# Performance work log

Hardware: AMD Instinct MI355X
Metric: run time of the kernel (lower is better)

Reference implementation:

```python
import jax, jax.numpy as jnp
import numpy as np

DIM_K = 128
MODEL_DIM = 1024
B, S = 8, 2048

def setup_inputs() -> dict:
    key = jax.random.key(0)
    k1, k2, k3, k4, k5, k6, k7 = jax.random.split(key, 7)
    return {
        "query": jax.random.normal(k1, (B, S, MODEL_DIM), dtype=jnp.float32),
        "key": jax.random.normal(k2, (B, S, MODEL_DIM), dtype=jnp.float32),
        "value": jax.random.normal(k3, (B, S, MODEL_DIM), dtype=jnp.float32),
        "mask": jax.random.randint(k4, (B, S, S), 0, 2, dtype=jnp.int32),
        # nn.Linear(model_dim, dim_k, bias=False): weight shape [dim_k, model_dim]
        "Wq": jax.random.normal(k5, (DIM_K, MODEL_DIM), dtype=jnp.float32) * (MODEL_DIM ** -0.5),
        "Wk": jax.random.normal(k6, (DIM_K, MODEL_DIM), dtype=jnp.float32) * (MODEL_DIM ** -0.5),
        "Wv": jax.random.normal(k7, (DIM_K, MODEL_DIM), dtype=jnp.float32) * (MODEL_DIM ** -0.5),
    }

def reference(query, key, value, mask, Wq, Wk, Wv):
    # projections: y = x @ W.T
    q = jnp.einsum('bsm,km->bsk', query, Wq)
    k = jnp.einsum('bsm,km->bsk', key, Wk)
    v = jnp.einsum('bsm,km->bsk', value, Wv)
    scale = 1.0 / jnp.sqrt(jnp.float32(DIM_K))
    pre_score = jnp.einsum('bqk,bsk->bqs', q, k) * scale  # [B,Sq,Sk]
    pre_score = jnp.where(mask == 0, jnp.float32(-1e9), pre_score)
    score = jax.nn.softmax(pre_score, axis=-1)
    return jnp.einsum('bqs,bsk->bqk', score, v)
```

## Files before the change

### kernel.cpp

```cpp
#include <hip/hip_runtime.h>
#include <hip/hip_bf16.h>

typedef __bf16 bf16x8 __attribute__((ext_vector_type(8)));
typedef float  f32x4  __attribute__((ext_vector_type(4)));

#define WS_Q  786432
#define WS_KP 2883584
#define WS_VP 4980736
#define WS_BF16_BYTES 14155776ull

__global__ __launch_bounds__(256) void wconv_kernel(
    const float* __restrict__ wq, const float* __restrict__ wk,
    const float* __restrict__ wv, __bf16* __restrict__ wpack)
{
    int i = blockIdx.x * 256 + threadIdx.x;
    int p = i >> 17, o = i & 131071;
    int c = o >> 3, j = o & 7;
    int l15 = c & 15, g = (c >> 4) & 3, nt = (c >> 6) & 7, ks = (c >> 9) & 1, kk = c >> 10;
    int col = nt * 16 + l15;
    int k = kk * 64 + ks * 32 + g * 8 + j;
    const float* src = (p == 0) ? wq : ((p == 1) ? wk : wv);
    float f = src[col * 1024 + k];
    if (p == 0) f *= (0.08838834764831845f * 1.44269504088896340736f);
    __bf16 h = (__bf16)f;
    __bf16 l = (__bf16)(f - (float)h);
    wpack[p * 262144 + o]          = h;
    wpack[p * 262144 + 131072 + o] = l;
}

__global__ __launch_bounds__(256, 4) void proj_kernel(
    const float* __restrict__ xq, const float* __restrict__ xk,
    const float* __restrict__ xv, const __bf16* __restrict__ wpack,
    __bf16* __restrict__ qws, __bf16* __restrict__ kpack, __bf16* __restrict__ vpack)
{
    const int p = blockIdx.y;
    const float* __restrict__ x = (p == 0) ? xq : ((p == 1) ? xk : xv);
    const __bf16* __restrict__ wf = wpack + p * 262144;

    const int mtile = blockIdx.x;
    const int m0 = mtile << 6;
    const int t = threadIdx.x;
    const int wv_ = t >> 6;
    const int lane = t & 63;
    const int l15 = lane & 15, g = lane >> 4;

    __shared__ __align__(16) __bf16 olds[9216];

    f32x4 acc[8];
#pragma unroll
    for (int nt = 0; nt < 8; ++nt) acc[nt] = (f32x4){0.f, 0.f, 0.f, 0.f};

    const float* xrow = x + (size_t)(m0 + wv_ * 16 + l15) * 1024 + g * 8;

    f32x4 a0 = *(const f32x4*)(xrow);
    f32x4 a1 = *(const f32x4*)(xrow + 4);
    f32x4 b0 = *(const f32x4*)(xrow + 32);
    f32x4 b1 = *(const f32x4*)(xrow + 36);

    for (int kk = 0; kk < 16; ++kk) {
        f32x4 na0, na1, nb0, nb1;
        if (kk < 15) {
            const float* nx = xrow + (kk + 1) * 64;
            na0 = *(const f32x4*)(nx);
            na1 = *(const f32x4*)(nx + 4);
            nb0 = *(const f32x4*)(nx + 32);
            nb1 = *(const f32x4*)(nx + 36);
        }
        bf16x8 ah0, ah1;
#pragma unroll
        for (int j = 0; j < 4; ++j) {
            ah0[j] = (__bf16)a0[j]; ah0[4 + j] = (__bf16)a1[j];
            ah1[j] = (__bf16)b0[j]; ah1[4 + j] = (__bf16)b1[j];
        }
        const __bf16* wb = wf + kk * 8192 + lane * 8;
#pragma unroll
        for (int nt = 0; nt < 8; ++nt) {
            bf16x8 bh0 = *(const bf16x8*)(wb + nt * 512);
            bf16x8 bl0 = *(const bf16x8*)(wb + nt * 512 + 131072);
            bf16x8 bh1 = *(const bf16x8*)(wb + nt * 512 + 4096);
            bf16x8 bl1 = *(const bf16x8*)(wb + nt * 512 + 4096 + 131072);
            acc[nt] = __builtin_amdgcn_mfma_f32_16x16x32_bf16(ah0, bh0, acc[nt], 0, 0, 0);
            acc[nt] = __builtin_amdgcn_mfma_f32_16x16x32_bf16(ah0, bl0, acc[nt], 0, 0, 0);
            acc[nt] = __builtin_amdgcn_mfma_f32_16x16x32_bf16(ah1, bh1, acc[nt], 0, 0, 0);
            acc[nt] = __builtin_amdgcn_mfma_f32_16x16x32_bf16(ah1, bl1, acc[nt], 0, 0, 0);
        }
        a0 = na0; a1 = na1; b0 = nb0; b1 = nb1;
    }

#pragma unroll
    for (int nt = 0; nt < 8; ++nt)
#pragma unroll
        for (int r = 0; r < 4; ++r) {
            int rowl = wv_ * 16 + g * 4 + r;
            int col = nt * 16 + l15;
            __bf16 v = (__bf16)acc[nt][r];
            if (p < 2) olds[rowl * 136 + col] = v;
            else       olds[col * 72 + rowl] = v;
        }
    __syncthreads();

    if (p == 0) {
#pragma unroll
        for (int i = 0; i < 4; ++i) {
            int idx = i * 256 + t;
            int row = idx >> 4, ck = idx & 15;
            bf16x8 v = *(const bf16x8*)(olds + row * 136 + ck * 8);
            *(bf16x8*)(qws + (size_t)(m0 + row) * 128 + ck * 8) = v;
        }
    } else if (p == 1) {
#pragma unroll
        for (int i = 0; i < 4; ++i) {
            int idx = i * 256 + t;
            int ks = idx >> 8, nt = (idx >> 6) & 3, ln = idx & 63;
            int gg = ln >> 4, ll = ln & 15;
            bf16x8 v = *(const bf16x8*)(olds + (nt * 16 + ll) * 136 + ks * 32 + gg * 8);
            *(bf16x8*)(kpack + ((size_t)mtile * 1024 + idx) * 8) = v;
        }
    } else {
#pragma unroll
        for (int i = 0; i < 4; ++i) {
            int idx = i * 256 + t;
            int ks2 = idx >> 9, nt2 = (idx >> 6) & 7, ln = idx & 63;
            int gg = ln >> 4, ll = ln & 15;
            bf16x8 v = *(const bf16x8*)(olds + (nt2 * 16 + ll) * 72 + ks2 * 32 + gg * 8);
            *(bf16x8*)(vpack + ((size_t)mtile * 1024 + idx) * 8) = v;
        }
    }
}

__global__ __launch_bounds__(256, 3) void flash_kernel(
    const __bf16* __restrict__ qws, const __bf16* __restrict__ kpack,
    const __bf16* __restrict__ vpack, const int* __restrict__ mask,
    float* __restrict__ out, float* __restrict__ part, float* __restrict__ mlbuf,
    int ktp)
{
    const int bb = blockIdx.x & 7;
    const int rest = blockIdx.x >> 3;
    const int mtile = rest & 31;
    const int jsplit = rest >> 5;
    const int sq0 = mtile << 6;
    const int t = threadIdx.x;
    const int wv_ = t >> 6;
    const int lane = t & 63;
    const int l15 = lane & 15, g = lane >> 4;

    __shared__ __align__(16) __bf16 psmem[4 * 1152];
    __bf16* plds = psmem + wv_ * 1152;

    bf16x8 qf[4];
    {
        const __bf16* qp = qws + ((size_t)(bb * 2048 + sq0 + wv_ * 16 + l15)) * 128 + g * 8;
#pragma unroll
        for (int ks = 0; ks < 4; ++ks) qf[ks] = *(const bf16x8*)(qp + ks * 32);
    }

    f32x4 o[8];
#pragma unroll
    for (int nt = 0; nt < 8; ++nt) o[nt] = (f32x4){0.f, 0.f, 0.f, 0.f};
    float m_run[4], l_run[4];
#pragma unroll
    for (int r = 0; r < 4; ++r) { m_run[r] = -__builtin_inff(); l_run[r] = 0.f; }

    const int* mbase = mask + ((size_t)(bb * 2048 + sq0 + wv_ * 16 + g * 4)) * 2048 + l15;
    const __bf16* kbase = kpack + ((size_t)(bb * 32) * 1024) * 8 + lane * 8;
    const __bf16* vbase = vpack + ((size_t)(bb * 32) * 1024) * 8 + lane * 8;

    const int kt_begin = jsplit * ktp, kt_end = kt_begin + ktp;
    for (int kt = kt_begin; kt < kt_end; ++kt) {
        const int n0 = kt << 6;

        int mv[4][4];
#pragma unroll
        for (int nt = 0; nt < 4; ++nt)
#pragma unroll
            for (int r = 0; r < 4; ++r)
                mv[nt][r] = mbase[(size_t)r * 2048 + n0 + nt * 16];

        const __bf16* kb = kbase + kt * 8192;
        f32x4 sf[4];
#pragma unroll
        for (int nt = 0; nt < 4; ++nt) sf[nt] = (f32x4){0.f, 0.f, 0.f, 0.f};
#pragma unroll
        for (int nt = 0; nt < 4; ++nt)
#pragma unroll
            for (int ks = 0; ks < 4; ++ks) {
                bf16x8 bfk = *(const bf16x8*)(kb + (ks * 4 + nt) * 512);
                sf[nt] = __builtin_amdgcn_mfma_f32_16x16x32_bf16(qf[ks], bfk, sf[nt], 0, 0, 0);
            }

        float mx[4], mnew[4], alpha[4], psum[4];
#pragma unroll
        for (int r = 0; r < 4; ++r)
            mx[r] = fmaxf(fmaxf(sf[0][r], sf[1][r]), fmaxf(sf[2][r], sf[3][r]));
#pragma unroll
        for (int off = 1; off < 16; off <<= 1)
#pragma unroll
            for (int r = 0; r < 4; ++r)
                mx[r] = fmaxf(mx[r], __shfl_xor(mx[r], off, 64));
#pragma unroll
        for (int r = 0; r < 4; ++r) {
            mnew[r] = fmaxf(m_run[r], mx[r]);
            alpha[r] = exp2f(m_run[r] - mnew[r]);
            psum[r] = 0.f;
        }
#pragma unroll
        for (int nt = 0; nt < 4; ++nt)
#pragma unroll
            for (int r = 0; r < 4; ++r) {
                float pv = exp2f(sf[nt][r] - mnew[r]);
                pv = mv[nt][r] ? pv : 0.f;
                psum[r] += pv;
                plds[(g * 4 + r) * 72 + nt * 16 + l15] = (__bf16)pv;
            }
#pragma unroll
        for (int off = 1; off < 16; off <<= 1)
#pragma unroll
            for (int r = 0; r < 4; ++r)
                psum[r] += __shfl_xor(psum[r], off, 64);
#pragma unroll
        for (int r = 0; r < 4; ++r) {
            l_run[r] = l_run[r] * alpha[r] + psum[r];
            m_run[r] = mnew[r];
        }
#pragma unroll
        for (int nt = 0; nt < 8; ++nt)
#pragma unroll
            for (int r = 0; r < 4; ++r) o[nt][r] *= alpha[r];

        bf16x8 pa[2];
#pragma unroll
        for (int ks2 = 0; ks2 < 2; ++ks2)
            pa[ks2] = *(const bf16x8*)(plds + l15 * 72 + ks2 * 32 + g * 8);

        const __bf16* vb = vbase + kt * 8192;
#pragma unroll
        for (int nt2 = 0; nt2 < 8; ++nt2)
#pragma unroll
            for (int ks2 = 0; ks2 < 2; ++ks2) {
                bf16x8 bfv = *(const bf16x8*)(vb + (ks2 * 8 + nt2) * 512);
                o[nt2] = __builtin_amdgcn_mfma_f32_16x16x32_bf16(pa[ks2], bfv, o[nt2], 0, 0, 0);
            }
    }

    if (part == nullptr) {
        float inv[4];
#pragma unroll
        for (int r = 0; r < 4; ++r) inv[r] = 1.0f / l_run[r];
#pragma unroll
        for (int nt2 = 0; nt2 < 8; ++nt2)
#pragma unroll
            for (int r = 0; r < 4; ++r)
                out[((size_t)(bb * 2048 + sq0 + wv_ * 16 + g * 4 + r)) * 128 + nt2 * 16 + l15] =
                    o[nt2][r] * inv[r];
    } else {
#pragma unroll
        for (int nt2 = 0; nt2 < 8; ++nt2)
#pragma unroll
            for (int r = 0; r < 4; ++r) {
                size_t rowg = (size_t)(bb * 2048 + sq0 + wv_ * 16 + g * 4 + r);
                part[((size_t)jsplit * 16384 + rowg) * 128 + nt2 * 16 + l15] = o[nt2][r];
            }
        if (l15 == 0) {
#pragma unroll
            for (int r = 0; r < 4; ++r) {
                size_t rowg = (size_t)(bb * 2048 + sq0 + wv_ * 16 + g * 4 + r);
                mlbuf[((size_t)jsplit * 16384 + rowg) * 2]     = m_run[r];
                mlbuf[((size_t)jsplit * 16384 + rowg) * 2 + 1] = l_run[r];
            }
        }
    }
}

__global__ __launch_bounds__(256) void merge_kernel(
    const float* __restrict__ part, const float* __restrict__ mlbuf,
    float* __restrict__ out, int J)
{
    int t = threadIdx.x;
    size_t row = (size_t)blockIdx.x * 8 + (t >> 5);
    int c = (t & 31) * 4;
    float mj[4];
    float m = -__builtin_inff();
    for (int j = 0; j < J; ++j) {
        mj[j] = mlbuf[((size_t)j * 16384 + row) * 2];
        m = fmaxf(m, mj[j]);
    }
    float l = 0.f;
    f32x4 acc = (f32x4){0.f, 0.f, 0.f, 0.f};
    for (int j = 0; j < J; ++j) {
        float w = exp2f(mj[j] - m);
        l += w * mlbuf[((size_t)j * 16384 + row) * 2 + 1];
        f32x4 v = *(const f32x4*)(part + ((size_t)j * 16384 + row) * 128 + c);
#pragma unroll
        for (int e = 0; e < 4; ++e) acc[e] += w * v[e];
    }
    float inv = 1.0f / l;
#pragma unroll
    for (int e = 0; e < 4; ++e) acc[e] *= inv;
    *(f32x4*)(out + row * 128 + c) = acc;
}

extern "C" void kernel_launch(void* const* d_in, const int* in_sizes, int n_in,
                              void* d_out, int out_size, void* d_ws, size_t ws_size,
                              hipStream_t stream)
{
    const float* query = (const float*)d_in[0];
    const float* key   = (const float*)d_in[1];
    const float* value = (const float*)d_in[2];
    const int*   mask  = (const int*)d_in[3];
    const float* Wq    = (const float*)d_in[4];
    const float* Wk    = (const float*)d_in[5];
    const float* Wv    = (const float*)d_in[6];
    float* out = (float*)d_out;

    __bf16* wpack = (__bf16*)d_ws;
    __bf16* qws = wpack + WS_Q;
    __bf16* kpack = wpack + WS_KP;
    __bf16* vpack = wpack + WS_VP;

    const size_t per_split = 16384ull * 128 * 4 + 16384ull * 8;
    int J = 1;
    if (ws_size >= WS_BF16_BYTES + 4 * per_split)      J = 4;
    else if (ws_size >= WS_BF16_BYTES + 2 * per_split) J = 2;
    float* part = (J > 1) ? (float*)((char*)d_ws + WS_BF16_BYTES) : nullptr;
    float* mlbuf = (J > 1) ? (part + (size_t)J * 16384 * 128) : nullptr;

    wconv_kernel<<<1536, 256, 0, stream>>>(Wq, Wk, Wv, wpack);
    proj_kernel<<<dim3(256, 3), 256, 0, stream>>>(query, key, value, wpack, qws, kpack, vpack);
    flash_kernel<<<256 * J, 256, 0, stream>>>(qws, kpack, vpack, mask, out, part, mlbuf, 32 / J);
    if (J > 1) merge_kernel<<<2048, 256, 0, stream>>>(part, mlbuf, out, J);
}
```

Before: 434.1 us.

## Stage projection weights in LDS with 2-row-tile waves; prefetch mask and K/V fragments

The projection kernel now runs two waves per block, each computing two 16-row M tiles. The split-bf16 weight slices are double-buffered through shared memory, so each weight fragment is reused across M tiles instead of re-read from global memory per wave. In the flash kernel, all K and V fragments for a tile are loaded into registers up front, and the mask for the next tile is prefetched, to hide load latency. The cost is higher register pressure in the flash kernel (the occupancy hint is dropped) and a barrier per half-K step in the projection.

```diff
diff --git a/kernel.cpp b/kernel.cpp
--- a/kernel.cpp
+++ b/kernel.cpp
@@ -28,7 +28,7 @@
     wpack[p * 262144 + 131072 + o] = l;
 }
 
-__global__ __launch_bounds__(256, 4) void proj_kernel(
+__global__ __launch_bounds__(128) void proj_kernel(
     const float* __restrict__ xq, const float* __restrict__ xk,
     const float* __restrict__ xv, const __bf16* __restrict__ wpack,
     __bf16* __restrict__ qws, __bf16* __restrict__ kpack, __bf16* __restrict__ vpack)
@@ -40,77 +40,112 @@
     const int mtile = blockIdx.x;
     const int m0 = mtile << 6;
     const int t = threadIdx.x;
-    const int wv_ = t >> 6;
+    const int w = t >> 6;
     const int lane = t & 63;
     const int l15 = lane & 15, g = lane >> 4;
 
+    __shared__ __align__(16) __bf16 wlds[2][8192];
     __shared__ __align__(16) __bf16 olds[9216];
 
-    f32x4 acc[8];
-#pragma unroll
-    for (int nt = 0; nt < 8; ++nt) acc[nt] = (f32x4){0.f, 0.f, 0.f, 0.f};
-
-    const float* xrow = x + (size_t)(m0 + wv_ * 16 + l15) * 1024 + g * 8;
-
-    f32x4 a0 = *(const f32x4*)(xrow);
-    f32x4 a1 = *(const f32x4*)(xrow + 4);
-    f32x4 b0 = *(const f32x4*)(xrow + 32);
-    f32x4 b1 = *(const f32x4*)(xrow + 36);
-
-    for (int kk = 0; kk < 16; ++kk) {
-        f32x4 na0, na1, nb0, nb1;
-        if (kk < 15) {
-            const float* nx = xrow + (kk + 1) * 64;
-            na0 = *(const f32x4*)(nx);
-            na1 = *(const f32x4*)(nx + 4);
-            nb0 = *(const f32x4*)(nx + 32);
-            nb1 = *(const f32x4*)(nx + 36);
-        }
-        bf16x8 ah0, ah1;
-#pragma unroll
-        for (int j = 0; j < 4; ++j) {
-            ah0[j] = (__bf16)a0[j]; ah0[4 + j] = (__bf16)a1[j];
-            ah1[j] = (__bf16)b0[j]; ah1[4 + j] = (__bf16)b1[j];
-        }
-        const __bf16* wb = wf + kk * 8192 + lane * 8;
+    f32x4 acc[2][8];
+#pragma unroll
+    for (int mt = 0; mt < 2; ++mt)
+#pragma unroll
+        for (int nt = 0; nt < 8; ++nt) acc[mt][nt] = (f32x4){0.f, 0.f, 0.f, 0.f};
+
+    const float* xb[2];
+    xb[0] = x + (size_t)(m0 + w * 32 + l15) * 1024 + g * 8;
+    xb[1] = xb[0] + 16 * 1024;
+
+    f32x4 xc[2][4], xn[2][4];
+#pragma unroll
+    for (int mt = 0; mt < 2; ++mt)
+#pragma unroll
+        for (int i = 0; i < 4; ++i)
+            xc[mt][i] = *(const f32x4*)(xb[mt] + (i >> 1) * 32 + (i & 1) * 4);
+
+    auto stage = [&](int hs, int buf) {
+#pragma unroll
+        for (int s = 0; s < 8; ++s) {
+            int seg = w * 8 + s;
+            const __bf16* src = wf + ((seg < 8) ? ((size_t)hs * 4096 + seg * 512)
+                                                : (131072ull + (size_t)hs * 4096 + (seg - 8) * 512))
+                                + lane * 8;
+            *(bf16x8*)(&wlds[buf][seg * 512 + lane * 8]) = *(const bf16x8*)src;
+        }
+    };
+
+    stage(0, 0);
+    __syncthreads();
+
+    for (int hs = 0; hs < 32; ++hs) {
+        const int buf = hs & 1 ^ 0;
+        const int kk = hs >> 1, ks = hs & 1;
+
+        if (hs < 31) stage(hs + 1, buf ^ 1);
+
+        if (ks == 0) {
+            int nkk = (kk < 15) ? kk + 1 : 0;
+#pragma unroll
+            for (int mt = 0; mt < 2; ++mt)
+#pragma unroll
+                for (int i = 0; i < 4; ++i)
+                    xn[mt][i] = *(const f32x4*)(xb[mt] + nkk * 64 + (i >> 1) * 32 + (i & 1) * 4);
+        }
+
+        bf16x8 ah[2];
+#pragma unroll
+        for (int mt = 0; mt < 2; ++mt)
+#pragma unroll
+            for (int e = 0; e < 8; ++e)
+                ah[mt][e] = (__bf16)xc[mt][ks * 2 + (e >> 2)][e & 3];
+
 #pragma unroll
         for (int nt = 0; nt < 8; ++nt) {
-            bf16x8 bh0 = *(const bf16x8*)(wb + nt * 512);
-            bf16x8 bl0 = *(const bf16x8*)(wb + nt * 512 + 131072);
-            bf16x8 bh1 = *(const bf16x8*)(wb + nt * 512 + 4096);
-            bf16x8 bl1 = *(const bf16x8*)(wb + nt * 512 + 4096 + 131072);
-            acc[nt] = __builtin_amdgcn_mfma_f32_16x16x32_bf16(ah0, bh0, acc[nt], 0, 0, 0);
-            acc[nt] = __builtin_amdgcn_mfma_f32_16x16x32_bf16(ah0, bl0, acc[nt], 0, 0, 0);
-            acc[nt] = __builtin_amdgcn_mfma_f32_16x16x32_bf16(ah1, bh1, acc[nt], 0, 0, 0);
-            acc[nt] = __builtin_amdgcn_mfma_f32_16x16x32_bf16(ah1, bl1, acc[nt], 0, 0, 0);
-        }
-        a0 = na0; a1 = na1; b0 = nb0; b1 = nb1;
-    }
-
-#pragma unroll
-    for (int nt = 0; nt < 8; ++nt)
-#pragma unroll
-        for (int r = 0; r < 4; ++r) {
-            int rowl = wv_ * 16 + g * 4 + r;
-            int col = nt * 16 + l15;
-            __bf16 v = (__bf16)acc[nt][r];
-            if (p < 2) olds[rowl * 136 + col] = v;
-            else       olds[col * 72 + rowl] = v;
-        }
+            bf16x8 bh = *(const bf16x8*)(&wlds[buf][nt * 512 + lane * 8]);
+            bf16x8 bl = *(const bf16x8*)(&wlds[buf][4096 + nt * 512 + lane * 8]);
+#pragma unroll
+            for (int mt = 0; mt < 2; ++mt) {
+                acc[mt][nt] = __builtin_amdgcn_mfma_f32_16x16x32_bf16(ah[mt], bh, acc[mt][nt], 0, 0, 0);
+                acc[mt][nt] = __builtin_amdgcn_mfma_f32_16x16x32_bf16(ah[mt], bl, acc[mt][nt], 0, 0, 0);
+            }
+        }
+
+        if (ks == 1) {
+#pragma unroll
+            for (int mt = 0; mt < 2; ++mt)
+#pragma unroll
+                for (int i = 0; i < 4; ++i) xc[mt][i] = xn[mt][i];
+        }
+        __syncthreads();
+    }
+
+#pragma unroll
+    for (int mt = 0; mt < 2; ++mt)
+#pragma unroll
+        for (int nt = 0; nt < 8; ++nt)
+#pragma unroll
+            for (int r = 0; r < 4; ++r) {
+                int rowl = w * 32 + mt * 16 + g * 4 + r;
+                int col = nt * 16 + l15;
+                __bf16 v = (__bf16)acc[mt][nt][r];
+                if (p < 2) olds[rowl * 136 + col] = v;
+                else       olds[col * 72 + rowl] = v;
+            }
     __syncthreads();
 
     if (p == 0) {
 #pragma unroll
-        for (int i = 0; i < 4; ++i) {
-            int idx = i * 256 + t;
+        for (int i = 0; i < 8; ++i) {
+            int idx = i * 128 + t;
             int row = idx >> 4, ck = idx & 15;
             bf16x8 v = *(const bf16x8*)(olds + row * 136 + ck * 8);
             *(bf16x8*)(qws + (size_t)(m0 + row) * 128 + ck * 8) = v;
         }
     } else if (p == 1) {
 #pragma unroll
-        for (int i = 0; i < 4; ++i) {
-            int idx = i * 256 + t;
+        for (int i = 0; i < 8; ++i) {
+            int idx = i * 128 + t;
             int ks = idx >> 8, nt = (idx >> 6) & 3, ln = idx & 63;
             int gg = ln >> 4, ll = ln & 15;
             bf16x8 v = *(const bf16x8*)(olds + (nt * 16 + ll) * 136 + ks * 32 + gg * 8);
@@ -118,8 +153,8 @@
         }
     } else {
 #pragma unroll
-        for (int i = 0; i < 4; ++i) {
-            int idx = i * 256 + t;
+        for (int i = 0; i < 8; ++i) {
+            int idx = i * 128 + t;
             int ks2 = idx >> 9, nt2 = (idx >> 6) & 7, ln = idx & 63;
             int gg = ln >> 4, ll = ln & 15;
             bf16x8 v = *(const bf16x8*)(olds + (nt2 * 16 + ll) * 72 + ks2 * 32 + gg * 8);
@@ -128,7 +163,7 @@
     }
 }
 
-__global__ __launch_bounds__(256, 3) void flash_kernel(
+__global__ __launch_bounds__(256) void flash_kernel(
     const __bf16* __restrict__ qws, const __bf16* __restrict__ kpack,
     const __bf16* __restrict__ vpack, const int* __restrict__ mask,
     float* __restrict__ out, float* __restrict__ part, float* __restrict__ mlbuf,
@@ -166,27 +201,41 @@
     const __bf16* vbase = vpack + ((size_t)(bb * 32) * 1024) * 8 + lane * 8;
 
     const int kt_begin = jsplit * ktp, kt_end = kt_begin + ktp;
+
+    int mv[4][4];
+#pragma unroll
+    for (int nt = 0; nt < 4; ++nt)
+#pragma unroll
+        for (int r = 0; r < 4; ++r)
+            mv[nt][r] = mbase[(size_t)r * 2048 + kt_begin * 64 + nt * 16];
+
     for (int kt = kt_begin; kt < kt_end; ++kt) {
-        const int n0 = kt << 6;
-
-        int mv[4][4];
+        const __bf16* kb = kbase + kt * 8192;
+        bf16x8 kfr[16];
+#pragma unroll
+        for (int i = 0; i < 16; ++i) kfr[i] = *(const bf16x8*)(kb + i * 512);
+
+        f32x4 sf[4];
+#pragma unroll
+        for (int nt = 0; nt < 4; ++nt) sf[nt] = (f32x4){0.f, 0.f, 0.f, 0.f};
 #pragma unroll
         for (int nt = 0; nt < 4; ++nt)
 #pragma unroll
+            for (int ks = 0; ks < 4; ++ks)
+                sf[nt] = __builtin_amdgcn_mfma_f32_16x16x32_bf16(qf[ks], kfr[ks * 4 + nt], sf[nt], 0, 0, 0);
+
+        const __bf16* vb = vbase + kt * 8192;
+        bf16x8 vfr[16];
+#pragma unroll
+        for (int i = 0; i < 16; ++i) vfr[i] = *(const bf16x8*)(vb + i * 512);
+
+        int ktn = (kt + 1 < kt_end) ? kt + 1 : kt_begin;
+        int mvn[4][4];
+#pragma unroll
+        for (int nt = 0; nt < 4; ++nt)
+#pragma unroll
             for (int r = 0; r < 4; ++r)
-                mv[nt][r] = mbase[(size_t)r * 2048 + n0 + nt * 16];
-
-        const __bf16* kb = kbase + kt * 8192;
-        f32x4 sf[4];
-#pragma unroll
-        for (int nt = 0; nt < 4; ++nt) sf[nt] = (f32x4){0.f, 0.f, 0.f, 0.f};
-#pragma unroll
-        for (int nt = 0; nt < 4; ++nt)
-#pragma unroll
-            for (int ks = 0; ks < 4; ++ks) {
-                bf16x8 bfk = *(const bf16x8*)(kb + (ks * 4 + nt) * 512);
-                sf[nt] = __builtin_amdgcn_mfma_f32_16x16x32_bf16(qf[ks], bfk, sf[nt], 0, 0, 0);
-            }
+                mvn[nt][r] = mbase[(size_t)r * 2048 + ktn * 64 + nt * 16];
 
         float mx[4], mnew[4], alpha[4], psum[4];
 #pragma unroll
@@ -232,14 +281,16 @@
         for (int ks2 = 0; ks2 < 2; ++ks2)
             pa[ks2] = *(const bf16x8*)(plds + l15 * 72 + ks2 * 32 + g * 8);
 
-        const __bf16* vb = vbase + kt * 8192;
 #pragma unroll
         for (int nt2 = 0; nt2 < 8; ++nt2)
 #pragma unroll
-            for (int ks2 = 0; ks2 < 2; ++ks2) {
-                bf16x8 bfv = *(const bf16x8*)(vb + (ks2 * 8 + nt2) * 512);
-                o[nt2] = __builtin_amdgcn_mfma_f32_16x16x32_bf16(pa[ks2], bfv, o[nt2], 0, 0, 0);
-            }
+            for (int ks2 = 0; ks2 < 2; ++ks2)
+                o[nt2] = __builtin_amdgcn_mfma_f32_16x16x32_bf16(pa[ks2], vfr[ks2 * 8 + nt2], o[nt2], 0, 0, 0);
+
+#pragma unroll
+        for (int nt = 0; nt < 4; ++nt)
+#pragma unroll
+            for (int r = 0; r < 4; ++r) mv[nt][r] = mvn[nt][r];
     }
 
     if (part == nullptr) {
@@ -287,11 +338,11 @@
     float l = 0.f;
     f32x4 acc = (f32x4){0.f, 0.f, 0.f, 0.f};
     for (int j = 0; j < J; ++j) {
-        float w = exp2f(mj[j] - m);
-        l += w * mlbuf[((size_t)j * 16384 + row) * 2 + 1];
+        float wgt = exp2f(mj[j] - m);
+        l += wgt * mlbuf[((size_t)j * 16384 + row) * 2 + 1];
         f32x4 v = *(const f32x4*)(part + ((size_t)j * 16384 + row) * 128 + c);
 #pragma unroll
-        for (int e = 0; e < 4; ++e) acc[e] += w * v[e];
+        for (int e = 0; e < 4; ++e) acc[e] += wgt * v[e];
     }
     float inv = 1.0f / l;
 #pragma unroll
@@ -325,7 +376,7 @@
     float* mlbuf = (J > 1) ? (part + (size_t)J * 16384 * 128) : nullptr;
 
     wconv_kernel<<<1536, 256, 0, stream>>>(Wq, Wk, Wv, wpack);
-    proj_kernel<<<dim3(256, 3), 256, 0, stream>>>(query, key, value, wpack, qws, kpack, vpack);
+    proj_kernel<<<dim3(256, 3), 128, 0, stream>>>(query, key, value, wpack, qws, kpack, vpack);
     flash_kernel<<<256 * J, 256, 0, stream>>>(qws, kpack, vpack, mask, out, part, mlbuf, 32 / J);
     if (J > 1) merge_kernel<<<2048, 256, 0, stream>>>(part, mlbuf, out, J);
 }
```

New measurement: 455.2 us. 4.9% more time.
